# Kernel tuning notes

Hardware: AMD Instinct MI355X
Metric: run time of the kernel (lower is better)

The kernel has to match this reference:

```python
import jax, jax.numpy as jnp
import numpy as np

N = 50000          # nodes
E = 800000         # edges (before self loops)
H = 4              # attention heads
C = 64             # per-head channels
D_IN = 256
NEG_ATT = 0.2      # GATConv attention LeakyReLU slope
NEG_ACT = 0.01     # nn.LeakyReLU default slope
EPS = 1e-5
MLP_DIMS = [64, 32, 16, 2]


def _gat_layer(x, src, dst, W, a_src, a_dst, b, concat):
    """PyG GATConv: gather -> segment-softmax over dst -> scatter-add."""
    n = x.shape[0]
    h = (x @ W).reshape(n, H, C)                       # [N,H,C]
    s = (h * a_src).sum(-1)                            # [N,H]
    d = (h * a_dst).sum(-1)                            # [N,H]
    e = jax.nn.leaky_relu(s[src] + d[dst], NEG_ATT)    # [E',H]
    m = jax.ops.segment_max(e, dst, num_segments=n)    # per-dst max (self loops -> no empty segs)
    w = jnp.exp(e - m[dst])
    den = jax.ops.segment_sum(w, dst, num_segments=n)
    alpha = w / den[dst]                               # [E',H]
    out = jax.ops.segment_sum(alpha[:, :, None] * h[src], dst, num_segments=n)  # [N,H,C]
    out = out.reshape(n, H * C) if concat else out.mean(axis=1)
    return out + b


def _graph_norm(x, w, b, a):
    mu = x.mean(axis=0, keepdims=True)
    y = x - a * mu
    var = (y * y).mean(axis=0, keepdims=True)
    return w * y * jax.lax.rsqrt(var + EPS) + b


def setup_inputs() -> dict:
    key = jax.random.key(0)
    ks = jax.random.split(key, 40)
    d = {
        'x': jax.random.normal(ks[0], (N, D_IN), dtype=jnp.float32),
        'edge_index': jax.random.randint(ks[1], (2, E), 0, N, dtype=jnp.int64),
    }
    dims_in = [D_IN, H * C, H * C]
    norm_dims = [H * C, H * C, C]
    k = 2
    for i in range(3):
        fan = dims_in[i]
        d[f'W{i}'] = jax.random.normal(ks[k], (fan, H * C), dtype=jnp.float32) / np.sqrt(fan); k += 1
        d[f'as{i}'] = jax.random.normal(ks[k], (H, C), dtype=jnp.float32) / np.sqrt(C); k += 1
        d[f'ad{i}'] = jax.random.normal(ks[k], (H, C), dtype=jnp.float32) / np.sqrt(C); k += 1
        d[f'b{i}'] = jnp.zeros((norm_dims[i],), dtype=jnp.float32)
        d[f'gw{i}'] = jnp.ones((norm_dims[i],), dtype=jnp.float32)
        d[f'gb{i}'] = jnp.zeros((norm_dims[i],), dtype=jnp.float32)
        d[f'ga{i}'] = jnp.ones((norm_dims[i],), dtype=jnp.float32)
    for j in range(3):
        fi, fo = MLP_DIMS[j], MLP_DIMS[j + 1]
        d[f'mW{j}'] = jax.random.normal(ks[k], (fi, fo), dtype=jnp.float32) / np.sqrt(fi); k += 1
        d[f'mb{j}'] = jnp.zeros((fo,), dtype=jnp.float32)
    return d


def reference(x, edge_index,
              W0, as0, ad0, b0, gw0, gb0, ga0,
              W1, as1, ad1, b1, gw1, gb1, ga1,
              W2, as2, ad2, b2, gw2, gb2, ga2,
              mW0, mb0, mW1, mb1, mW2, mb2):
    n = x.shape[0]
    loop = jnp.arange(n, dtype=edge_index.dtype)
    src = jnp.concatenate([edge_index[0], loop])   # add self loops (PyG default)
    dst = jnp.concatenate([edge_index[1], loop])

    h = _gat_layer(x, src, dst, W0, as0, ad0, b0, concat=True)
    h = jax.nn.leaky_relu(_graph_norm(h, gw0, gb0, ga0), NEG_ACT)
    h = _gat_layer(h, src, dst, W1, as1, ad1, b1, concat=True)
    h = jax.nn.leaky_relu(_graph_norm(h, gw1, gb1, ga1), NEG_ACT)
    h = _gat_layer(h, src, dst, W2, as2, ad2, b2, concat=False)
    h = jax.nn.leaky_relu(_graph_norm(h, gw2, gb2, ga2), NEG_ACT)

    h = jax.nn.relu(h @ mW0 + mb0)
    h = jax.nn.relu(h @ mW1 + mb1)
    return h @ mW2 + mb2
```

## Files before the change

kernel.cpp:

```cpp
#include <hip/hip_runtime.h>

#define NN 50000
#define EE 800000
#define ET 850000
#define HH 4
#define CC 64
#define FDIM 256

#define SCAN_BLK 512
#define SCAN_NB ((NN + SCAN_BLK - 1) / SCAN_BLK)

typedef unsigned short ushort;
typedef __bf16 bf16x8 __attribute__((ext_vector_type(8)));
typedef float floatx4 __attribute__((ext_vector_type(4)));
typedef ushort ushort8v __attribute__((ext_vector_type(8)));
typedef ushort ushort4v __attribute__((ext_vector_type(4)));
struct ushort4s { ushort x, y, z, w; };

__device__ __forceinline__ ushort f2bf(float f) {
  union { float f; unsigned u; } v; v.f = f;
  unsigned r = v.u + 0x7fffu + ((v.u >> 16) & 1u);
  return (ushort)(r >> 16);
}
__device__ __forceinline__ float bf2f(ushort u) {
  return __uint_as_float(((unsigned)u) << 16);
}

__device__ __forceinline__ int get_edge(const void* p, int is64, long long idx) {
  if (is64) return (int)((const long long*)p)[idx];
  return ((const int*)p)[idx];
}

__global__ void degree_kernel(const void* eidx, int is64, int* deg) {
  int k = blockIdx.x * blockDim.x + threadIdx.x;
  if (k >= ET) return;
  int dst = (k < EE) ? get_edge(eidx, is64, (long long)EE + k) : (k - EE);
  atomicAdd(&deg[dst], 1);
}

__global__ __launch_bounds__(SCAN_BLK) void scan1_kernel(const int* __restrict__ deg,
                                                         int* __restrict__ rowptr,
                                                         int* __restrict__ bsum) {
  __shared__ int sm[SCAN_BLK];
  int t = threadIdx.x;
  int i = blockIdx.x * SCAN_BLK + t;
  int v = (i < NN) ? deg[i] : 0;
  sm[t] = v;
  __syncthreads();
#pragma unroll
  for (int o = 1; o < SCAN_BLK; o <<= 1) {
    int u = (t >= o) ? sm[t - o] : 0;
    __syncthreads();
    sm[t] += u;
    __syncthreads();
  }
  if (i < NN) rowptr[i] = sm[t] - v;
  if (t == SCAN_BLK - 1) bsum[blockIdx.x] = sm[t];
}

__global__ __launch_bounds__(128) void scan2_kernel(const int* __restrict__ bsum,
                                                    int* __restrict__ boff,
                                                    int* __restrict__ rowptr) {
  __shared__ int sm[128];
  int t = threadIdx.x;
  int v = (t < SCAN_NB) ? bsum[t] : 0;
  sm[t] = v;
  __syncthreads();
#pragma unroll
  for (int o = 1; o < 128; o <<= 1) {
    int u = (t >= o) ? sm[t - o] : 0;
    __syncthreads();
    sm[t] += u;
    __syncthreads();
  }
  if (t < SCAN_NB) boff[t] = sm[t] - v;
  if (t == 0) rowptr[NN] = ET;
}

__global__ __launch_bounds__(SCAN_BLK) void scan3_kernel(int* __restrict__ rowptr,
                                                         int* __restrict__ cursor,
                                                         const int* __restrict__ boff) {
  int i = blockIdx.x * SCAN_BLK + threadIdx.x;
  if (i >= NN) return;
  int v = rowptr[i] + boff[blockIdx.x];
  rowptr[i] = v;
  cursor[i] = v;
}

__global__ void fill_kernel(const void* eidx, int is64, int* cursor, int* csr_src) {
  int k = blockIdx.x * blockDim.x + threadIdx.x;
  if (k >= ET) return;
  int src, dst;
  if (k < EE) {
    src = get_edge(eidx, is64, k);
    dst = get_edge(eidx, is64, (long long)EE + k);
  } else {
    src = dst = k - EE;
  }
  int pos = atomicAdd(&cursor[dst], 1);
  csr_src[pos] = src;
}

__global__ void conv_w_kernel(const float* __restrict__ W0, const float* __restrict__ W1,
                              const float* __restrict__ W2,
                              ushort* __restrict__ T0, ushort* __restrict__ T1,
                              ushort* __restrict__ T2) {
  const float* W = (blockIdx.y == 0) ? W0 : (blockIdx.y == 1) ? W1 : W2;
  ushort* Wt = (blockIdx.y == 0) ? T0 : (blockIdx.y == 1) ? T1 : T2;
  int idx = blockIdx.x * 256 + threadIdx.x;
  int k = idx >> 8, n = idx & 255;
  Wt[n * 256 + k] = f2bf(W[idx]);
}

template <int MODE>
__global__ __launch_bounds__(256) void gemm_bf16(const void* __restrict__ Ap,
                                                 const ushort* __restrict__ Bt,
                                                 ushort* __restrict__ C,
                                                 const float* __restrict__ as_,
                                                 const float* __restrict__ ad_,
                                                 float* __restrict__ s_arr,
                                                 float* __restrict__ d_arr,
                                                 const float* __restrict__ colsum,
                                                 const float* __restrict__ colsumsq,
                                                 const float* __restrict__ ga,
                                                 const float* __restrict__ gw,
                                                 const float* __restrict__ gb) {
  __shared__ ushort As[2 * 512];
  __shared__ ushort Bs[16 * 512];
  __shared__ float scs[FDIM], shs[FDIM];
  int tid = threadIdx.x, w = tid >> 6, l = tid & 63;
  int brow0 = blockIdx.x * 32;
  int lm = l & 15, lk = (l >> 4) * 8;
  int s_sub = tid >> 7;
  int within = tid & 127;
  int arow = brow0 + s_sub * 16 + ((within >> 1) & 15);
  arow = min(arow, NN - 1);
  int kbase = ((within >> 5) << 3) + ((within & 1) << 2);
  size_t aoff = (size_t)arow * 256 + kbase;
  int aldst = s_sub * 512 + within * 4;
  const ushort* bg[4];
#pragma unroll
  for (int j = 0; j < 4; j++)
    bg[j] = Bt + (size_t)((4 * w + j) * 16 + lm) * 256 + lk;

  if constexpr (MODE == 1) {
    const float invn = 1.0f / (float)NN;
    float mu = colsum[tid] * invn;
    float ex2 = colsumsq[tid] * invn;
    float a = ga[tid];
    float var = fmaxf(ex2 - (2.f * a - a * a) * mu * mu, 0.f);
    float s = gw[tid] * rsqrtf(var + 1e-5f);
    scs[tid] = s;
    shs[tid] = gb[tid] - s * a * mu;
    __syncthreads();
  }

  floatx4 acc[2][4];
#pragma unroll
  for (int i = 0; i < 2; i++)
#pragma unroll
    for (int j = 0; j < 4; j++) acc[i][j] = floatx4{0.f, 0.f, 0.f, 0.f};

  for (int k0 = 0; k0 < 256; k0 += 32) {
    ushort4v av;
    if constexpr (MODE == 0) {
      float4 u = *(const float4*)((const float*)Ap + aoff + k0);
      av = ushort4v{f2bf(u.x), f2bf(u.y), f2bf(u.z), f2bf(u.w)};
    } else {
      ushort4v r = *(const ushort4v*)((const ushort*)Ap + aoff + k0);
      int kb = k0 + kbase;
#pragma unroll
      for (int j = 0; j < 4; j++) {
        float y = fmaf(scs[kb + j], bf2f(r[j]), shs[kb + j]);
        y = fmaxf(y, 0.01f * y);
        av[j] = f2bf(y);
      }
    }
    ushort8v b0 = *(const ushort8v*)(bg[0] + k0);
    ushort8v b1 = *(const ushort8v*)(bg[1] + k0);
    ushort8v b2 = *(const ushort8v*)(bg[2] + k0);
    ushort8v b3 = *(const ushort8v*)(bg[3] + k0);
    *(ushort4v*)&As[aldst] = av;
    *(ushort8v*)&Bs[(4 * w + 0) * 512 + l * 8] = b0;
    *(ushort8v*)&Bs[(4 * w + 1) * 512 + l * 8] = b1;
    *(ushort8v*)&Bs[(4 * w + 2) * 512 + l * 8] = b2;
    *(ushort8v*)&Bs[(4 * w + 3) * 512 + l * 8] = b3;
    __syncthreads();
    bf16x8 af[2], bfr[4];
    af[0] = *(const bf16x8*)&As[l * 8];
    af[1] = *(const bf16x8*)&As[512 + l * 8];
#pragma unroll
    for (int j = 0; j < 4; j++) bfr[j] = *(const bf16x8*)&Bs[(4 * w + j) * 512 + l * 8];
#pragma unroll
    for (int i = 0; i < 2; i++)
#pragma unroll
      for (int j = 0; j < 4; j++)
        acc[i][j] = __builtin_amdgcn_mfma_f32_16x16x32_bf16(af[i], bfr[j], acc[i][j], 0, 0, 0);
    __syncthreads();
  }

  int quad = l >> 4;
#pragma unroll
  for (int i = 0; i < 2; i++) {
    int rr0 = brow0 + i * 16 + quad * 4;
#pragma unroll
    for (int j = 0; j < 4; j++) {
      int col = w * 64 + j * 16 + lm;
#pragma unroll
      for (int r = 0; r < 4; r++) {
        int row = rr0 + r;
        if (row < NN) C[(size_t)row * 256 + col] = f2bf(acc[i][j][r]);
      }
    }
  }
  float asv[4], adv[4];
#pragma unroll
  for (int j = 0; j < 4; j++) {
    int col = w * 64 + j * 16 + lm;
    asv[j] = as_[col];
    adv[j] = ad_[col];
  }
#pragma unroll
  for (int i = 0; i < 2; i++) {
#pragma unroll
    for (int r = 0; r < 4; r++) {
      float sp = acc[i][0][r] * asv[0] + acc[i][1][r] * asv[1] +
                 acc[i][2][r] * asv[2] + acc[i][3][r] * asv[3];
      float dp = acc[i][0][r] * adv[0] + acc[i][1][r] * adv[1] +
                 acc[i][2][r] * adv[2] + acc[i][3][r] * adv[3];
      sp += __shfl_xor(sp, 1); dp += __shfl_xor(dp, 1);
      sp += __shfl_xor(sp, 2); dp += __shfl_xor(dp, 2);
      sp += __shfl_xor(sp, 4); dp += __shfl_xor(dp, 4);
      sp += __shfl_xor(sp, 8); dp += __shfl_xor(dp, 8);
      if (lm == 0) {
        int row = brow0 + i * 16 + quad * 4 + r;
        if (row < NN) {
          s_arr[row * HH + w] = sp;
          d_arr[row * HH + w] = dp;
        }
      }
    }
  }
}

template <bool CONCAT>
__global__ __launch_bounds__(256) void agg_kernel(const ushort* __restrict__ hb,
                                                  const float* __restrict__ s_arr,
                                                  const float* __restrict__ d_arr,
                                                  const int* __restrict__ rowptr,
                                                  const int* __restrict__ csr_src,
                                                  const float* __restrict__ bias,
                                                  void* __restrict__ outp) {
  int w = __builtin_amdgcn_readfirstlane(threadIdx.x >> 6);
  int l = threadIdx.x & 63;
  int head = l >> 4;
  int n = blockIdx.x * 4 + w;
  int beg = rowptr[n], end = rowptr[n + 1];
  float dh = d_arr[n * HH + head];
  float a0 = 0.f, a1 = 0.f, a2 = 0.f, a3 = 0.f, den = 0.f;

  int i = beg;
  for (; i + 16 <= end; i += 16) {
    int ss[16];
#pragma unroll
    for (int t = 0; t < 16; t++) ss[t] = csr_src[i + t];
    float ee[16];
#pragma unroll
    for (int t = 0; t < 16; t++) ee[t] = s_arr[ss[t] * HH + head];
    ushort4s hh[16];
#pragma unroll
    for (int t = 0; t < 16; t++)
      hh[t] = *(const ushort4s*)(hb + (unsigned)(ss[t] * FDIM + l * 4));
#pragma unroll
    for (int t = 0; t < 16; t++) {
      float e = ee[t] + dh;
      e = (e > 0.f) ? e : 0.2f * e;
      float wt = __expf(e);
      den += wt;
      a0 = fmaf(wt, bf2f(hh[t].x), a0);
      a1 = fmaf(wt, bf2f(hh[t].y), a1);
      a2 = fmaf(wt, bf2f(hh[t].z), a2);
      a3 = fmaf(wt, bf2f(hh[t].w), a3);
    }
  }
  for (; i + 8 <= end; i += 8) {
    int ss[8];
#pragma unroll
    for (int t = 0; t < 8; t++) ss[t] = csr_src[i + t];
    float ee[8];
#pragma unroll
    for (int t = 0; t < 8; t++) ee[t] = s_arr[ss[t] * HH + head];
    ushort4s hh[8];
#pragma unroll
    for (int t = 0; t < 8; t++)
      hh[t] = *(const ushort4s*)(hb + (unsigned)(ss[t] * FDIM + l * 4));
#pragma unroll
    for (int t = 0; t < 8; t++) {
      float e = ee[t] + dh;
      e = (e > 0.f) ? e : 0.2f * e;
      float wt = __expf(e);
      den += wt;
      a0 = fmaf(wt, bf2f(hh[t].x), a0);
      a1 = fmaf(wt, bf2f(hh[t].y), a1);
      a2 = fmaf(wt, bf2f(hh[t].z), a2);
      a3 = fmaf(wt, bf2f(hh[t].w), a3);
    }
  }
  for (; i + 4 <= end; i += 4) {
    int ss[4];
#pragma unroll
    for (int t = 0; t < 4; t++) ss[t] = csr_src[i + t];
    float ee[4];
#pragma unroll
    for (int t = 0; t < 4; t++) ee[t] = s_arr[ss[t] * HH + head];
    ushort4s hh[4];
#pragma unroll
    for (int t = 0; t < 4; t++)
      hh[t] = *(const ushort4s*)(hb + (unsigned)(ss[t] * FDIM + l * 4));
#pragma unroll
    for (int t = 0; t < 4; t++) {
      float e = ee[t] + dh;
      e = (e > 0.f) ? e : 0.2f * e;
      float wt = __expf(e);
      den += wt;
      a0 = fmaf(wt, bf2f(hh[t].x), a0);
      a1 = fmaf(wt, bf2f(hh[t].y), a1);
      a2 = fmaf(wt, bf2f(hh[t].z), a2);
      a3 = fmaf(wt, bf2f(hh[t].w), a3);
    }
  }
  for (; i < end; i++) {
    int s0 = csr_src[i];
    float e0 = s_arr[s0 * HH + head] + dh;
    ushort4s h0 = *(const ushort4s*)(hb + (unsigned)(s0 * FDIM + l * 4));
    e0 = (e0 > 0.f) ? e0 : 0.2f * e0;
    float w0 = __expf(e0);
    den += w0;
    a0 = fmaf(w0, bf2f(h0.x), a0); a1 = fmaf(w0, bf2f(h0.y), a1);
    a2 = fmaf(w0, bf2f(h0.z), a2); a3 = fmaf(w0, bf2f(h0.w), a3);
  }
  float inv = 1.0f / den;
  float r0 = a0 * inv, r1 = a1 * inv, r2 = a2 * inv, r3 = a3 * inv;

  if (CONCAT) {
    float4 bv = ((const float4*)bias)[l];
    ushort4s o;
    o.x = f2bf(r0 + bv.x); o.y = f2bf(r1 + bv.y);
    o.z = f2bf(r2 + bv.z); o.w = f2bf(r3 + bv.w);
    ((ushort4s*)outp)[(unsigned)(n * 64 + l)] = o;
  } else {
    r0 += __shfl_xor(r0, 16); r1 += __shfl_xor(r1, 16);
    r2 += __shfl_xor(r2, 16); r3 += __shfl_xor(r3, 16);
    r0 += __shfl_xor(r0, 32); r1 += __shfl_xor(r1, 32);
    r2 += __shfl_xor(r2, 32); r3 += __shfl_xor(r3, 32);
    if (l < 16) {
      float4 bv = ((const float4*)bias)[l];
      float4 o;
      o.x = 0.25f * r0 + bv.x; o.y = 0.25f * r1 + bv.y;
      o.z = 0.25f * r2 + bv.z; o.w = 0.25f * r3 + bv.w;
      ((float4*)outp)[(unsigned)(n * 16 + l)] = o;
    }
  }
}

__global__ __launch_bounds__(256) void norm_reduce_bf(const ushort* __restrict__ xin,
                                                      float* colsum, float* colsumsq) {
  __shared__ float4 sm1[256], sm2[256];
  int t = threadIdx.x;
  int c4 = (t & 63) * 4;
  int rl = t >> 6;
  int r0 = blockIdx.x * 128;
  int r1 = min(NN, r0 + 128);
  float s0 = 0.f, s1 = 0.f, s2 = 0.f, s3 = 0.f;
  float q0 = 0.f, q1 = 0.f, q2 = 0.f, q3 = 0.f;
  for (int r = r0 + rl; r < r1; r += 4) {
    ushort4s v = *(const ushort4s*)(xin + (size_t)r * FDIM + c4);
    float f0 = bf2f(v.x), f1 = bf2f(v.y), f2 = bf2f(v.z), f3 = bf2f(v.w);
    s0 += f0; q0 += f0 * f0;
    s1 += f1; q1 += f1 * f1;
    s2 += f2; q2 += f2 * f2;
    s3 += f3; q3 += f3 * f3;
  }
  sm1[t] = float4{s0, s1, s2, s3};
  sm2[t] = float4{q0, q1, q2, q3};
  __syncthreads();
  if (t < 64) {
    float4 a = sm1[t], b = sm1[t + 64], c = sm1[t + 128], d = sm1[t + 192];
    atomicAdd(&colsum[c4 + 0], a.x + b.x + c.x + d.x);
    atomicAdd(&colsum[c4 + 1], a.y + b.y + c.y + d.y);
    atomicAdd(&colsum[c4 + 2], a.z + b.z + c.z + d.z);
    atomicAdd(&colsum[c4 + 3], a.w + b.w + c.w + d.w);
    float4 e = sm2[t], f = sm2[t + 64], g = sm2[t + 128], h = sm2[t + 192];
    atomicAdd(&colsumsq[c4 + 0], e.x + f.x + g.x + h.x);
    atomicAdd(&colsumsq[c4 + 1], e.y + f.y + g.y + h.y);
    atomicAdd(&colsumsq[c4 + 2], e.z + f.z + g.z + h.z);
    atomicAdd(&colsumsq[c4 + 3], e.w + f.w + g.w + h.w);
  }
}

__global__ __launch_bounds__(256) void norm_reduce_f32(const float* __restrict__ xin,
                                                       float* colsum, float* colsumsq) {
  int f = threadIdx.x & (CC - 1);
  int rl = threadIdx.x / CC;
  int r0 = blockIdx.x * 128;
  int r1 = min(NN, r0 + 128);
  float s1 = 0.f, s2 = 0.f;
  for (int r = r0 + rl; r < r1; r += 4) {
    float v = xin[(size_t)r * CC + f];
    s1 += v; s2 += v * v;
  }
  atomicAdd(&colsum[f], s1);
  atomicAdd(&colsumsq[f], s2);
}

__global__ __launch_bounds__(256) void mlp_kernel(const float* __restrict__ xin,
                                                  const float* __restrict__ colsum,
                                                  const float* __restrict__ colsumsq,
                                                  const float* __restrict__ ga,
                                                  const float* __restrict__ gw,
                                                  const float* __restrict__ gb,
                                                  const float* mW0, const float* mb0,
                                                  const float* mW1, const float* mb1,
                                                  const float* mW2, const float* mb2,
                                                  float* __restrict__ out) {
  __shared__ float W0s[64 * 32];
  __shared__ float W1s[32 * 16];
  __shared__ float W2s[16 * 2];
  __shared__ float b0s[32], b1s[16], b2s[2];
  __shared__ float sc[CC], sh[CC];
  int t = threadIdx.x;
  for (int i = t; i < 2048; i += 256) W0s[i] = mW0[i];
  for (int i = t; i < 512; i += 256) W1s[i] = mW1[i];
  if (t < 32) { W2s[t] = mW2[t]; b0s[t] = mb0[t]; }
  if (t < 16) b1s[t] = mb1[t];
  if (t < 2) b2s[t] = mb2[t];
  if (t < CC) {
    const float invn = 1.0f / (float)NN;
    float mu = colsum[t] * invn;
    float ex2 = colsumsq[t] * invn;
    float a = ga[t];
    float var = fmaxf(ex2 - (2.f * a - a * a) * mu * mu, 0.f);
    float s = gw[t] * rsqrtf(var + 1e-5f);
    sc[t] = s; sh[t] = gb[t] - s * a * mu;
  }
  __syncthreads();
  int node = blockIdx.x * 256 + t;
  if (node >= NN) return;
  float in[64];
  const float* xr = xin + (size_t)node * 64;
#pragma unroll
  for (int k = 0; k < 64; k++) {
    float y = sc[k] * xr[k] + sh[k];
    in[k] = (y > 0.f) ? y : 0.01f * y;
  }
  float h1[32];
#pragma unroll
  for (int j = 0; j < 32; j++) h1[j] = b0s[j];
#pragma unroll
  for (int k = 0; k < 64; k++) {
    float v = in[k];
#pragma unroll
    for (int j = 0; j < 32; j++) h1[j] += v * W0s[k * 32 + j];
  }
#pragma unroll
  for (int j = 0; j < 32; j++) h1[j] = fmaxf(h1[j], 0.f);
  float h2[16];
#pragma unroll
  for (int j = 0; j < 16; j++) h2[j] = b1s[j];
#pragma unroll
  for (int k = 0; k < 32; k++) {
    float v = h1[k];
#pragma unroll
    for (int j = 0; j < 16; j++) h2[j] += v * W1s[k * 16 + j];
  }
#pragma unroll
  for (int j = 0; j < 16; j++) h2[j] = fmaxf(h2[j], 0.f);
  float o0 = b2s[0], o1 = b2s[1];
#pragma unroll
  for (int k = 0; k < 16; k++) {
    o0 += h2[k] * W2s[k * 2 + 0];
    o1 += h2[k] * W2s[k * 2 + 1];
  }
  out[(size_t)node * 2 + 0] = o0;
  out[(size_t)node * 2 + 1] = o1;
}

extern "C" void kernel_launch(void* const* d_in, const int* in_sizes, int n_in,
                              void* d_out, int out_size, void* d_ws, size_t ws_size,
                              hipStream_t stream) {
  const float* x = (const float*)d_in[0];
  const void* ei = d_in[1];
  const float* W[3]   = {(const float*)d_in[2],  (const float*)d_in[9],  (const float*)d_in[16]};
  const float* as_[3] = {(const float*)d_in[3],  (const float*)d_in[10], (const float*)d_in[17]};
  const float* ad_[3] = {(const float*)d_in[4],  (const float*)d_in[11], (const float*)d_in[18]};
  const float* b_[3]  = {(const float*)d_in[5],  (const float*)d_in[12], (const float*)d_in[19]};
  const float* gw[3]  = {(const float*)d_in[6],  (const float*)d_in[13], (const float*)d_in[20]};
  const float* gb[3]  = {(const float*)d_in[7],  (const float*)d_in[14], (const float*)d_in[21]};
  const float* ga[3]  = {(const float*)d_in[8],  (const float*)d_in[15], (const float*)d_in[22]};
  const float* mW0 = (const float*)d_in[23];
  const float* mb0 = (const float*)d_in[24];
  const float* mW1 = (const float*)d_in[25];
  const float* mb1 = (const float*)d_in[26];
  const float* mW2 = (const float*)d_in[27];
  const float* mb2 = (const float*)d_in[28];
  float* out = (float*)d_out;

  int is64 = (in_sizes[1] == (int)(2u * EE * 8u)) ? 1 : 0;

  char* ws = (char*)d_ws;
  size_t off = 0;
  auto take = [&](size_t bytes) -> char* {
    char* p = ws + off;
    off = (off + bytes + 255) & ~(size_t)255;
    return p;
  };
  ushort* hb    = (ushort*)take((size_t)NN * FDIM * 2);
  ushort* aggb  = (ushort*)take((size_t)NN * FDIM * 2);
  float* bufD   = (float*)take((size_t)NN * CC * 4);
  ushort* Wt[3];
  for (int i = 0; i < 3; i++) Wt[i] = (ushort*)take((size_t)256 * 256 * 2);
  float* s_arr  = (float*)take((size_t)NN * HH * 4);
  float* d_arr  = (float*)take((size_t)NN * HH * 4);
  char* zbase   = (char*)take(0);
  int* deg      = (int*)take((size_t)NN * 4);
  float* cs[3];
  for (int i = 0; i < 3; i++) cs[i] = (float*)take(2048);
  size_t zlen   = (size_t)(((char*)cs[2] + 2048) - zbase);
  int* cursor   = (int*)take((size_t)NN * 4);
  int* rowptr   = (int*)take((size_t)(NN + 1) * 4);
  int* csr_src  = (int*)take((size_t)ET * 4);
  int* bsum     = (int*)take(512);
  int* boff     = (int*)take(512);

  hipMemsetAsync(zbase, 0, zlen, stream);

  degree_kernel<<<(ET + 255) / 256, 256, 0, stream>>>(ei, is64, deg);
  scan1_kernel<<<SCAN_NB, SCAN_BLK, 0, stream>>>(deg, rowptr, bsum);
  scan2_kernel<<<1, 128, 0, stream>>>(bsum, boff, rowptr);
  scan3_kernel<<<SCAN_NB, SCAN_BLK, 0, stream>>>(rowptr, cursor, boff);
  fill_kernel<<<(ET + 255) / 256, 256, 0, stream>>>(ei, is64, cursor, csr_src);

  conv_w_kernel<<<dim3(256, 3), 256, 0, stream>>>(W[0], W[1], W[2], Wt[0], Wt[1], Wt[2]);

  int ggrid = (NN + 31) / 32;
  for (int L = 0; L < 3; L++) {
    if (L == 0)
      gemm_bf16<0><<<ggrid, 256, 0, stream>>>((const void*)x, Wt[0], hb,
                                              as_[0], ad_[0], s_arr, d_arr,
                                              nullptr, nullptr, nullptr, nullptr, nullptr);
    else
      gemm_bf16<1><<<ggrid, 256, 0, stream>>>((const void*)aggb, Wt[L], hb,
                                              as_[L], ad_[L], s_arr, d_arr,
                                              cs[L - 1], cs[L - 1] + 256,
                                              ga[L - 1], gw[L - 1], gb[L - 1]);
    if (L < 2) {
      agg_kernel<true><<<NN / 4, 256, 0, stream>>>(hb, s_arr, d_arr, rowptr, csr_src, b_[L], aggb);
      norm_reduce_bf<<<(NN + 127) / 128, 256, 0, stream>>>(aggb, cs[L], cs[L] + 256);
    } else {
      agg_kernel<false><<<NN / 4, 256, 0, stream>>>(hb, s_arr, d_arr, rowptr, csr_src, b_[L], bufD);
      norm_reduce_f32<<<(NN + 127) / 128, 256, 0, stream>>>(bufD, cs[2], cs[2] + 256);
    }
  }
  mlp_kernel<<<(NN + 255) / 256, 256, 0, stream>>>(bufD, cs[2], cs[2] + 256,
                                                   ga[2], gw[2], gb[2],
                                                   mW0, mb0, mW1, mb1, mW2, mb2, out);
}
```

Before: 705.1 us.

## Load GEMM fragments directly from global memory, dropping LDS staging and barriers

The bf16 MFMA GEMM no longer stages A and B tiles through shared memory with two barriers per k-step. Each wave now loads its A and B fragments straight from global memory into registers in MFMA operand layout, and the k-loop is fully unrolled. This removes the LDS round trips and synchronisation, but all four waves now load the same A rows redundantly from global memory and cache, and register pressure from the unrolled loop rises.

```diff
diff --git a/kernel.cpp b/kernel.cpp
--- a/kernel.cpp
+++ b/kernel.cpp
@@ -14,7 +14,6 @@
 typedef __bf16 bf16x8 __attribute__((ext_vector_type(8)));
 typedef float floatx4 __attribute__((ext_vector_type(4)));
 typedef ushort ushort8v __attribute__((ext_vector_type(8)));
-typedef ushort ushort4v __attribute__((ext_vector_type(4)));
 struct ushort4s { ushort x, y, z, w; };
 
 __device__ __forceinline__ ushort f2bf(float f) {
@@ -125,23 +124,18 @@
                                                  const float* __restrict__ ga,
                                                  const float* __restrict__ gw,
                                                  const float* __restrict__ gb) {
-  __shared__ ushort As[2 * 512];
-  __shared__ ushort Bs[16 * 512];
   __shared__ float scs[FDIM], shs[FDIM];
   int tid = threadIdx.x, w = tid >> 6, l = tid & 63;
   int brow0 = blockIdx.x * 32;
   int lm = l & 15, lk = (l >> 4) * 8;
-  int s_sub = tid >> 7;
-  int within = tid & 127;
-  int arow = brow0 + s_sub * 16 + ((within >> 1) & 15);
-  arow = min(arow, NN - 1);
-  int kbase = ((within >> 5) << 3) + ((within & 1) << 2);
-  size_t aoff = (size_t)arow * 256 + kbase;
-  int aldst = s_sub * 512 + within * 4;
-  const ushort* bg[4];
+  int ar0 = min(brow0 + lm, NN - 1);
+  int ar1 = min(brow0 + 16 + lm, NN - 1);
+  size_t abase0 = (size_t)ar0 * 256 + lk;
+  size_t abase1 = (size_t)ar1 * 256 + lk;
+  const ushort* bp[4];
 #pragma unroll
   for (int j = 0; j < 4; j++)
-    bg[j] = Bt + (size_t)((4 * w + j) * 16 + lm) * 256 + lk;
+    bp[j] = Bt + (size_t)(w * 64 + j * 16 + lm) * 256 + lk;
 
   if constexpr (MODE == 1) {
     const float invn = 1.0f / (float)NN;
@@ -161,42 +155,59 @@
 #pragma unroll
     for (int j = 0; j < 4; j++) acc[i][j] = floatx4{0.f, 0.f, 0.f, 0.f};
 
+#pragma unroll
   for (int k0 = 0; k0 < 256; k0 += 32) {
-    ushort4v av;
+    bf16x8 af0, af1;
     if constexpr (MODE == 0) {
-      float4 u = *(const float4*)((const float*)Ap + aoff + k0);
-      av = ushort4v{f2bf(u.x), f2bf(u.y), f2bf(u.z), f2bf(u.w)};
+      const float* A = (const float*)Ap;
+      float4 u0 = *(const float4*)(A + abase0 + k0);
+      float4 u1 = *(const float4*)(A + abase0 + k0 + 4);
+      float4 v0 = *(const float4*)(A + abase1 + k0);
+      float4 v1 = *(const float4*)(A + abase1 + k0 + 4);
+      ushort8v a0{f2bf(u0.x), f2bf(u0.y), f2bf(u0.z), f2bf(u0.w),
+                  f2bf(u1.x), f2bf(u1.y), f2bf(u1.z), f2bf(u1.w)};
+      ushort8v a1{f2bf(v0.x), f2bf(v0.y), f2bf(v0.z), f2bf(v0.w),
+                  f2bf(v1.x), f2bf(v1.y), f2bf(v1.z), f2bf(v1.w)};
+      af0 = *(bf16x8*)&a0;
+      af1 = *(bf16x8*)&a1;
     } else {
-      ushort4v r = *(const ushort4v*)((const ushort*)Ap + aoff + k0);
-      int kb = k0 + kbase;
+      const ushort* A = (const ushort*)Ap;
+      ushort8v r0 = *(const ushort8v*)(A + abase0 + k0);
+      ushort8v r1 = *(const ushort8v*)(A + abase1 + k0);
+      int k = k0 + lk;
+      float4 sc0 = *(const float4*)&scs[k];
+      float4 sc1 = *(const float4*)&scs[k + 4];
+      float4 sh0 = *(const float4*)&shs[k];
+      float4 sh1 = *(const float4*)&shs[k + 4];
+      ushort8v a0, a1;
 #pragma unroll
       for (int j = 0; j < 4; j++) {
-        float y = fmaf(scs[kb + j], bf2f(r[j]), shs[kb + j]);
-        y = fmaxf(y, 0.01f * y);
-        av[j] = f2bf(y);
+        float y0 = fmaf(((const float*)&sc0)[j], bf2f(r0[j]), ((const float*)&sh0)[j]);
+        float y1 = fmaf(((const float*)&sc1)[j], bf2f(r0[j + 4]), ((const float*)&sh1)[j]);
+        float z0 = fmaf(((const float*)&sc0)[j], bf2f(r1[j]), ((const float*)&sh0)[j]);
+        float z1 = fmaf(((const float*)&sc1)[j], bf2f(r1[j + 4]), ((const float*)&sh1)[j]);
+        y0 = fmaxf(y0, 0.01f * y0);
+        y1 = fmaxf(y1, 0.01f * y1);
+        z0 = fmaxf(z0, 0.01f * z0);
+        z1 = fmaxf(z1, 0.01f * z1);
+        a0[j] = f2bf(y0); a0[j + 4] = f2bf(y1);
+        a1[j] = f2bf(z0); a1[j + 4] = f2bf(z1);
       }
-    }
-    ushort8v b0 = *(const ushort8v*)(bg[0] + k0);
-    ushort8v b1 = *(const ushort8v*)(bg[1] + k0);
-    ushort8v b2 = *(const ushort8v*)(bg[2] + k0);
-    ushort8v b3 = *(const ushort8v*)(bg[3] + k0);
-    *(ushort4v*)&As[aldst] = av;
-    *(ushort8v*)&Bs[(4 * w + 0) * 512 + l * 8] = b0;
-    *(ushort8v*)&Bs[(4 * w + 1) * 512 + l * 8] = b1;
-    *(ushort8v*)&Bs[(4 * w + 2) * 512 + l * 8] = b2;
-    *(ushort8v*)&Bs[(4 * w + 3) * 512 + l * 8] = b3;
-    __syncthreads();
-    bf16x8 af[2], bfr[4];
-    af[0] = *(const bf16x8*)&As[l * 8];
-    af[1] = *(const bf16x8*)&As[512 + l * 8];
-#pragma unroll
-    for (int j = 0; j < 4; j++) bfr[j] = *(const bf16x8*)&Bs[(4 * w + j) * 512 + l * 8];
-#pragma unroll
-    for (int i = 0; i < 2; i++)
-#pragma unroll
-      for (int j = 0; j < 4; j++)
-        acc[i][j] = __builtin_amdgcn_mfma_f32_16x16x32_bf16(af[i], bfr[j], acc[i][j], 0, 0, 0);
-    __syncthreads();
+      af0 = *(bf16x8*)&a0;
+      af1 = *(bf16x8*)&a1;
+    }
+    bf16x8 bf0 = *(const bf16x8*)(bp[0] + k0);
+    bf16x8 bf1 = *(const bf16x8*)(bp[1] + k0);
+    bf16x8 bf2 = *(const bf16x8*)(bp[2] + k0);
+    bf16x8 bf3 = *(const bf16x8*)(bp[3] + k0);
+    acc[0][0] = __builtin_amdgcn_mfma_f32_16x16x32_bf16(af0, bf0, acc[0][0], 0, 0, 0);
+    acc[1][0] = __builtin_amdgcn_mfma_f32_16x16x32_bf16(af1, bf0, acc[1][0], 0, 0, 0);
+    acc[0][1] = __builtin_amdgcn_mfma_f32_16x16x32_bf16(af0, bf1, acc[0][1], 0, 0, 0);
+    acc[1][1] = __builtin_amdgcn_mfma_f32_16x16x32_bf16(af1, bf1, acc[1][1], 0, 0, 0);
+    acc[0][2] = __builtin_amdgcn_mfma_f32_16x16x32_bf16(af0, bf2, acc[0][2], 0, 0, 0);
+    acc[1][2] = __builtin_amdgcn_mfma_f32_16x16x32_bf16(af1, bf2, acc[1][2], 0, 0, 0);
+    acc[0][3] = __builtin_amdgcn_mfma_f32_16x16x32_bf16(af0, bf3, acc[0][3], 0, 0, 0);
+    acc[1][3] = __builtin_amdgcn_mfma_f32_16x16x32_bf16(af1, bf3, acc[1][3], 0, 0, 0);
   }
 
   int quad = l >> 4;
```

Result: slower. 732.1 us (+3.8%).
